# Kernel tuning notes

Hardware: AMD Instinct MI355X
Metric: run time of the kernel (lower is better)

## Reference

```python
import jax, jax.numpy as jnp
import numpy as np

NUM_HEADS = 16
D_MODEL = 1024
NUM_LAYERS = 4
VOCAB = 32000
SEQ_LEN = 1024
BATCH = 4
EPS = 1e-6


def position_embedding(seq_len, d_model):
    pos = jnp.arange(seq_len, dtype=jnp.float32)[:, None]
    i = jnp.arange(d_model, dtype=jnp.float32)[None, :]
    # faithful to source: angle_rates = 1 / (1/10000)^(2*(i//2)/d) = 10000^(2*(i//2)/d)
    angle_rates = jnp.power(10000.0, 2.0 * jnp.floor(i / 2.0) / float(d_model))
    ang = pos * angle_rates  # [S, D]
    return jnp.concatenate([jnp.sin(ang[:, 0::2]), jnp.cos(ang[:, 1::2])], axis=-1)[None]  # [1,S,D]


def layer_norm(x, g, b):
    m = jnp.mean(x, axis=-1, keepdims=True)
    v = jnp.mean(jnp.square(x - m), axis=-1, keepdims=True)
    return (x - m) * jax.lax.rsqrt(v + EPS) * g + b


def setup_inputs() -> dict:
    key = jax.random.key(0)
    ks = jax.random.split(key, 20)
    L, D = NUM_LAYERS, D_MODEL
    s = 0.02
    inp = {
        "x": jax.random.randint(ks[0], (BATCH, SEQ_LEN), 0, VOCAB, dtype=jnp.int32),
        "mask": jnp.zeros((BATCH, 1, 1, SEQ_LEN), dtype=jnp.float32),
        "emb": jax.random.normal(ks[1], (VOCAB, D), dtype=jnp.float32) * s,
        "wq": jax.random.normal(ks[2], (L, D, D), dtype=jnp.float32) * s,
        "bq": jnp.zeros((L, D), dtype=jnp.float32),
        "wk": jax.random.normal(ks[3], (L, D, D), dtype=jnp.float32) * s,
        "bk": jnp.zeros((L, D), dtype=jnp.float32),
        "wv": jax.random.normal(ks[4], (L, D, D), dtype=jnp.float32) * s,
        "bv": jnp.zeros((L, D), dtype=jnp.float32),
        "wo": jax.random.normal(ks[5], (L, D, D), dtype=jnp.float32) * s,
        "bo": jnp.zeros((L, D), dtype=jnp.float32),
        "wf": jax.random.normal(ks[6], (L, D, D), dtype=jnp.float32) * s,
        "bf": jnp.zeros((L, D), dtype=jnp.float32),
        "g1": jnp.ones((L, D), dtype=jnp.float32),
        "b1": jnp.zeros((L, D), dtype=jnp.float32),
        "g2": jnp.ones((L, D), dtype=jnp.float32),
        "b2": jnp.zeros((L, D), dtype=jnp.float32),
    }
    return inp


def encoder_forward(x, mask, emb, wq, bq, wk, bk, wv, bv, wo, bo, wf, bf, g1, b1, g2, b2):
    B, S = x.shape
    D = emb.shape[1]
    H = NUM_HEADS
    dh = D // H
    h = emb[x] * jnp.sqrt(jnp.float32(D))  # [B,S,D]
    h = h + position_embedding(S, D)[:, :S, :]

    def split_heads(t):  # [B,S,D] -> [B,H,S,dh]
        return t.reshape(B, S, H, dh).transpose(0, 2, 1, 3)

    for l in range(wq.shape[0]):
        q = split_heads(h @ wq[l] + bq[l])
        k = split_heads(h @ wk[l] + bk[l])
        v = split_heads(h @ wv[l] + bv[l])
        scores = jnp.einsum("bhqd,bhkd->bhqk", q, k) / jnp.sqrt(jnp.float32(dh))
        scores = scores + mask * -1e9
        w = jax.nn.softmax(scores, axis=-1)
        ctx = jnp.einsum("bhqk,bhkd->bhqd", w, v)  # [B,H,S,dh]
        ctx = ctx.transpose(0, 2, 1, 3).reshape(B, S, D)
        attn_out = ctx @ wo[l] + bo[l]
        h = layer_norm(h + attn_out, g1[l], b1[l])
        ff = h @ wf[l] + bf[l]
        h = layer_norm(h + ff, g2[l], b2[l])
    return h


def reference(x, mask, emb, wq, bq, wk, bk, wv, bv, wo, bo, wf, bf, g1, b1, g2, b2):
    return encoder_forward(x, mask, emb, wq, bq, wk, bk, wv, bv, wo, bo, wf, bf, g1, b1, g2, b2)
```

## Files before the change

### kernel.cpp

```cpp
#include <hip/hip_runtime.h>
#include <hip/hip_bf16.h>
#include <math.h>

typedef __hip_bfloat16 bf16;
typedef unsigned int u32;
typedef __attribute__((ext_vector_type(8))) short short8;
typedef __attribute__((ext_vector_type(4))) float f32x4;


#define ATT_LDK 72
#define PS_LD  72

typedef __attribute__((address_space(3))) u32 lds_u32;
typedef const __attribute__((address_space(1))) u32 glb_u32;
static __device__ __forceinline__ void g2l16(const void* g, void* l) {
    __builtin_amdgcn_global_load_lds((glb_u32*)g, (lds_u32*)l, 16, 0, 0);
}

static __device__ __forceinline__ unsigned short bf16bits(float f) {
    bf16 h = __float2bfloat16(f);
    return *(unsigned short*)&h;
}

__global__ __launch_bounds__(256) void wprep_kernel(
    const float* __restrict__ wq, const float* __restrict__ wk,
    const float* __restrict__ wv, const float* __restrict__ wo,
    const float* __restrict__ wf, bf16* __restrict__ wt_all)
{
    __shared__ bf16 tile[64][ATT_LDK];
    const int z = blockIdx.z;
    const int l = z / 5, f = z % 5;
    const float* src = (f == 0) ? wq : (f == 1) ? wk : (f == 2) ? wv : (f == 3) ? wo : wf;
    src += (size_t)l * 1024 * 1024;
    bf16* dst = wt_all + ((size_t)l * 5 + f) * 1024 * 1024;

    const int k0 = blockIdx.x * 64, n0 = blockIdx.y * 64;
    const int t = threadIdx.x;
#pragma unroll
    for (int rr = 0; rr < 4; ++rr) {
        int slot = t + rr * 256;
        int r = slot >> 4, c = slot & 15;
        float4 v = *(const float4*)(src + (size_t)(k0 + r) * 1024 + n0 + c * 4);
        tile[c * 4 + 0][r] = __float2bfloat16(v.x);
        tile[c * 4 + 1][r] = __float2bfloat16(v.y);
        tile[c * 4 + 2][r] = __float2bfloat16(v.z);
        tile[c * 4 + 3][r] = __float2bfloat16(v.w);
    }
    __syncthreads();
#pragma unroll
    for (int rr = 0; rr < 2; ++rr) {
        int slot = t + rr * 256;
        int n = slot >> 3, c = slot & 7;
        *(uint4*)(dst + (size_t)(n0 + n) * 1024 + k0 + c * 8) = *(const uint4*)&tile[n][c * 8];
    }
}

__global__ void bias_stack_kernel(const float* __restrict__ bq, const float* __restrict__ bk,
                                  const float* __restrict__ bv, float* __restrict__ bqkv,
                                  float* __restrict__ rate)
{
    int i = blockIdx.x * 256 + threadIdx.x;
    if (i < 1024) {
        int m = (i < 512) ? i : (i - 512);
        float ex = (float)(2 * m) * (1.0f / 1024.0f);
        rate[i] = (float)pow(10000.0, (double)ex);
    }
    if (i < 4 * 3072) {
        int l = i / 3072, c = i % 3072;
        int fam = c >> 10, cc = c & 1023;
        const float* s = (fam == 0) ? bq : (fam == 1) ? bk : bv;
        bqkv[i] = s[l * 1024 + cc];
    }
}

__global__ __launch_bounds__(256) void pe_kernel(const float* __restrict__ rate,
                                                 float* __restrict__ pe)
{
    int idx = blockIdx.x * 256 + threadIdx.x;
    int d0 = (idx & 255) * 4;
    int s = idx >> 8;
    float out[4];
#pragma unroll
    for (int j = 0; j < 4; ++j) {
        int d = d0 + j;
        float ang = (float)s * rate[d];
        double a = (double)ang;
        out[j] = (d < 512) ? (float)sin(a) : (float)cos(a);
    }
    *(float4*)(pe + (size_t)s * 1024 + d0) = *(float4*)out;
}

__global__ __launch_bounds__(256) void embed_kernel(
    const int* __restrict__ x, const float* __restrict__ emb,
    const float* __restrict__ pe,
    float* __restrict__ hf, bf16* __restrict__ hb)
{
    int idx = blockIdx.x * 256 + threadIdx.x;
    int d0 = (idx & 255) * 4;
    int row = idx >> 8;
    int s = row & 1023;
    int tok = x[row];
    float4 e = *(const float4*)(emb + (size_t)tok * 1024 + d0);
    float4 p = *(const float4*)(pe + (size_t)s * 1024 + d0);
    float out[4] = {e.x * 32.0f + p.x, e.y * 32.0f + p.y,
                    e.z * 32.0f + p.z, e.w * 32.0f + p.w};
    *(float4*)(hf + (size_t)row * 1024 + d0) = *(float4*)out;
    unsigned short pk[4];
#pragma unroll
    for (int j = 0; j < 4; ++j) pk[j] = bf16bits(out[j]);
    *(uint2*)(hb + (size_t)row * 1024 + d0) = *(uint2*)pk;
}

__global__ __launch_bounds__(256, 3) void gemm_bt_kernel(
    const bf16* __restrict__ A, const bf16* __restrict__ Bt,
    const float* __restrict__ bias,
    bf16* __restrict__ Cb, bf16* __restrict__ VtOut,
    int M, int N, int K)
{
    __shared__ bf16 As[2][128 * 32];
    __shared__ bf16 Bs[2][128 * 32];
    __shared__ bf16 Cst[4][16 * PS_LD];
    const int t = threadIdx.x;
    const int lane = t & 63, wave = t >> 6;
    const int wr = wave >> 1, wc = wave & 1;
    const int lidx = lane & 15, quad = lane >> 4;
    const int m0 = blockIdx.x * 128, n0 = blockIdx.y * 128;

    f32x4 acc[4][4];
#pragma unroll
    for (int i = 0; i < 4; ++i)
#pragma unroll
        for (int j = 0; j < 4; ++j) acc[i][j] = (f32x4){0.f, 0.f, 0.f, 0.f};

    const int r0 = wave * 32;
    const int rloc = lane >> 2;
    const int csw = ((lane & 3) ^ ((lane >> 3) & 3)) * 8;
    const bf16* Abase = A  + (size_t)(m0 + r0 + rloc) * K + csw;
    const bf16* Bbase = Bt + (size_t)(n0 + r0 + rloc) * K + csw;
    const int lofs = r0 * 32;
    const int aslot = (quad ^ ((lidx >> 1) & 3)) * 8;

    g2l16(Abase,                  &As[0][lofs]);
    g2l16(Abase + 16 * (size_t)K, &As[0][lofs + 16 * 32]);
    g2l16(Bbase,                  &Bs[0][lofs]);
    g2l16(Bbase + 16 * (size_t)K, &Bs[0][lofs + 16 * 32]);

    for (int k0 = 0; k0 < K; k0 += 32) {
        __syncthreads();
        const int cur = (k0 >> 5) & 1;
        if (k0 + 32 < K) {
            const int kn = k0 + 32;
            g2l16(Abase + kn,                  &As[cur ^ 1][lofs]);
            g2l16(Abase + kn + 16 * (size_t)K, &As[cur ^ 1][lofs + 16 * 32]);
            g2l16(Bbase + kn,                  &Bs[cur ^ 1][lofs]);
            g2l16(Bbase + kn + 16 * (size_t)K, &Bs[cur ^ 1][lofs + 16 * 32]);
        }

        short8 af[4], bfr[4];
#pragma unroll
        for (int i = 0; i < 4; ++i)
            af[i] = *(const short8*)(&As[cur][(wr * 64 + i * 16 + lidx) * 32 + aslot]);
#pragma unroll
        for (int j = 0; j < 4; ++j)
            bfr[j] = *(const short8*)(&Bs[cur][(wc * 64 + j * 16 + lidx) * 32 + aslot]);
#pragma unroll
        for (int i = 0; i < 4; ++i)
#pragma unroll
            for (int j = 0; j < 4; ++j)
                acc[i][j] = __builtin_amdgcn_mfma_f32_16x16x32_bf16(af[i], bfr[j], acc[i][j], 0, 0, 0);
    }

    float bvj[4];
#pragma unroll
    for (int j = 0; j < 4; ++j)
        bvj[j] = bias ? bias[n0 + wc * 64 + j * 16 + lidx] : 0.0f;

    if (VtOut && n0 >= 2048) {
        const int bidx = m0 >> 10;
        const int s_base = (m0 & 1023) + wr * 64 + quad * 4;
        const int d_base = (n0 - 2048) + wc * 64;
#pragma unroll
        for (int i = 0; i < 4; ++i)
#pragma unroll
            for (int j = 0; j < 4; ++j) {
                unsigned short pk[4];
#pragma unroll
                for (int r = 0; r < 4; ++r)
                    pk[r] = bf16bits(acc[i][j][r] + bvj[j]);
                bf16* dst = VtOut + ((size_t)bidx * 1024 + d_base + j * 16 + lidx) * 1024
                            + s_base + i * 16;
                *(uint2*)dst = *(const uint2*)pk;
            }
    } else {
        const int row16 = lane >> 2, c4 = lane & 3;
#pragma unroll
        for (int i = 0; i < 4; ++i) {
#pragma unroll
            for (int j = 0; j < 4; ++j)
#pragma unroll
                for (int r = 0; r < 4; ++r)
                    Cst[wave][(quad * 4 + r) * PS_LD + j * 16 + lidx] =
                        __float2bfloat16(acc[i][j][r] + bvj[j]);
            bf16* dst = Cb + (size_t)(m0 + wr * 64 + i * 16 + row16) * N + n0 + wc * 64;
            const bf16* srcr = &Cst[wave][row16 * PS_LD];
#pragma unroll
            for (int h = 0; h < 2; ++h)
                *(uint4*)(dst + (c4 + 4 * h) * 8) = *(const uint4*)(srcr + (c4 + 4 * h) * 8);
        }
    }
}

__global__ __launch_bounds__(256, 4) void gemm64_kernel(
    const bf16* __restrict__ A, const bf16* __restrict__ Bt,
    const float* __restrict__ bias, const float* __restrict__ resid,
    float* __restrict__ Cf,
    int M, int N, int K)
{
    __shared__ bf16 As[2][64 * 32];
    __shared__ bf16 Bs[2][128 * 32];
    const int t = threadIdx.x;
    const int lane = t & 63, wave = t >> 6;
    const int wr = wave >> 1, wc = wave & 1;
    const int lidx = lane & 15, quad = lane >> 4;
    const int m0 = blockIdx.x * 64, n0 = blockIdx.y * 128;

    f32x4 acc[2][4];
#pragma unroll
    for (int i = 0; i < 2; ++i)
#pragma unroll
        for (int j = 0; j < 4; ++j) acc[i][j] = (f32x4){0.f, 0.f, 0.f, 0.f};

    const int rloc = lane >> 2;
    const int csw = ((lane & 3) ^ ((lane >> 3) & 3)) * 8;
    const bf16* Abase = A  + (size_t)(m0 + wave * 16 + rloc) * K + csw;
    const bf16* Bbase = Bt + (size_t)(n0 + wave * 32 + rloc) * K + csw;
    const int alofs = wave * 16 * 32;
    const int blofs = wave * 32 * 32;
    const int aslot = (quad ^ ((lidx >> 1) & 3)) * 8;

    g2l16(Abase,                  &As[0][alofs]);
    g2l16(Bbase,                  &Bs[0][blofs]);
    g2l16(Bbase + 16 * (size_t)K, &Bs[0][blofs + 16 * 32]);

    for (int k0 = 0; k0 < K; k0 += 32) {
        __syncthreads();
        const int cur = (k0 >> 5) & 1;
        if (k0 + 32 < K) {
            const int kn = k0 + 32;
            g2l16(Abase + kn,                  &As[cur ^ 1][alofs]);
            g2l16(Bbase + kn,                  &Bs[cur ^ 1][blofs]);
            g2l16(Bbase + kn + 16 * (size_t)K, &Bs[cur ^ 1][blofs + 16 * 32]);
        }

        short8 af[2], bfr[4];
#pragma unroll
        for (int i = 0; i < 2; ++i)
            af[i] = *(const short8*)(&As[cur][(wr * 32 + i * 16 + lidx) * 32 + aslot]);
#pragma unroll
        for (int j = 0; j < 4; ++j)
            bfr[j] = *(const short8*)(&Bs[cur][(wc * 64 + j * 16 + lidx) * 32 + aslot]);
#pragma unroll
        for (int i = 0; i < 2; ++i)
#pragma unroll
            for (int j = 0; j < 4; ++j)
                acc[i][j] = __builtin_amdgcn_mfma_f32_16x16x32_bf16(af[i], bfr[j], acc[i][j], 0, 0, 0);
    }

#pragma unroll
    for (int i = 0; i < 2; ++i)
#pragma unroll
        for (int j = 0; j < 4; ++j) {
            int col = n0 + wc * 64 + j * 16 + lidx;
            float bv = bias[col];
#pragma unroll
            for (int r = 0; r < 4; ++r) {
                int rowg = m0 + wr * 32 + i * 16 + quad * 4 + r;
                Cf[(size_t)rowg * N + col] =
                    acc[i][j][r] + bv + resid[(size_t)rowg * N + col];
            }
        }
}

__global__ __launch_bounds__(512, 4) void attention_kernel(
    const bf16* __restrict__ QKV,
    const bf16* __restrict__ Vt,
    const float* __restrict__ mask,
    bf16* __restrict__ ctx)
{
    __shared__ bf16 Ks[2][64 * 64];
    __shared__ bf16 Vs[2][64 * 64];
    __shared__ bf16 Ps[8][16 * PS_LD];

    const int t = threadIdx.x, lane = t & 63, wave = t >> 6;
    const int quad = lane >> 4, lidx = lane & 15;
    const int b = blockIdx.x >> 4, hh = blockIdx.x & 15;
    const int q0 = blockIdx.y * 128 + wave * 16;

    const int r8 = lane >> 3;
    const int gc = ((lane & 7) ^ r8) * 8;
    const bf16* kg0 = QKV + (size_t)(b * 1024 + wave * 8 + r8) * 3072 + 1024 + hh * 64 + gc;
    const bf16* vg0 = Vt  + (size_t)(b * 1024 + hh * 64 + wave * 8 + r8) * 1024 + gc;
    const int lofs = wave * 8 * 64;

    short8 qf[2];
    {
        const bf16* qp = QKV + (size_t)(b * 1024 + q0 + lidx) * 3072 + hh * 64;
        qf[0] = *(const short8*)(qp + quad * 8);
        qf[1] = *(const short8*)(qp + 32 + quad * 8);
    }

    f32x4 Oacc[4];
#pragma unroll
    for (int nt = 0; nt < 4; ++nt) Oacc[nt] = (f32x4){0.f, 0.f, 0.f, 0.f};
    float psum[4] = {0.f, 0.f, 0.f, 0.f};

    const int fslot = lidx & 7;

    g2l16(kg0, &Ks[0][lofs]);
    g2l16(vg0, &Vs[0][lofs]);

    for (int kt = 0; kt < 16; ++kt) {
        __syncthreads();
        const int cur = kt & 1;
        if (kt < 15) {
            g2l16(kg0 + (size_t)(kt + 1) * 64 * 3072, &Ks[cur ^ 1][lofs]);
            g2l16(vg0 + (kt + 1) * 64,                &Vs[cur ^ 1][lofs]);
        }

        f32x4 sacc[4];
#pragma unroll
        for (int nt = 0; nt < 4; ++nt) sacc[nt] = (f32x4){0.f, 0.f, 0.f, 0.f};
#pragma unroll
        for (int kk = 0; kk < 2; ++kk)
#pragma unroll
            for (int nt = 0; nt < 4; ++nt) {
                short8 kf = *(const short8*)(&Ks[cur][(nt * 16 + lidx) * 64 + (((kk * 4 + quad) ^ fslot) * 8)]);
                sacc[nt] = __builtin_amdgcn_mfma_f32_16x16x32_bf16(qf[kk], kf, sacc[nt], 0, 0, 0);
            }

#pragma unroll
        for (int nt = 0; nt < 4; ++nt) {
            float mv = mask[b * 1024 + kt * 64 + nt * 16 + lidx] * -1e9f;
#pragma unroll
            for (int r = 0; r < 4; ++r) {
                float p = __expf(sacc[nt][r] * 0.125f + mv);
                sacc[nt][r] = p;
                psum[r] += p;
            }
        }

#pragma unroll
        for (int nt = 0; nt < 4; ++nt)
#pragma unroll
            for (int r = 0; r < 4; ++r)
                Ps[wave][(quad * 4 + r) * PS_LD + nt * 16 + lidx] = __float2bfloat16(sacc[nt][r]);

#pragma unroll
        for (int kk = 0; kk < 2; ++kk) {
            short8 pf = *(const short8*)(&Ps[wave][lidx * PS_LD + kk * 32 + quad * 8]);
#pragma unroll
            for (int nt = 0; nt < 4; ++nt) {
                short8 vf = *(const short8*)(&Vs[cur][(nt * 16 + lidx) * 64 + (((kk * 4 + quad) ^ fslot) * 8)]);
                Oacc[nt] = __builtin_amdgcn_mfma_f32_16x16x32_bf16(pf, vf, Oacc[nt], 0, 0, 0);
            }
        }
    }

#pragma unroll
    for (int off = 1; off < 16; off <<= 1)
#pragma unroll
        for (int r = 0; r < 4; ++r)
            psum[r] += __shfl_xor(psum[r], off, 64);
    float linv[4];
#pragma unroll
    for (int r = 0; r < 4; ++r) linv[r] = 1.0f / psum[r];

#pragma unroll
    for (int nt = 0; nt < 4; ++nt)
#pragma unroll
        for (int r = 0; r < 4; ++r)
            Ps[wave][(quad * 4 + r) * PS_LD + nt * 16 + lidx] = __float2bfloat16(Oacc[nt][r] * linv[r]);

    const int row16 = lane >> 2, c4 = lane & 3;
    bf16* dst = ctx + (size_t)(b * 1024 + q0 + row16) * 1024 + hh * 64;
    const bf16* srcr = &Ps[wave][row16 * PS_LD];
#pragma unroll
    for (int h = 0; h < 2; ++h)
        *(uint4*)(dst + (c4 + 4 * h) * 8) = *(const uint4*)(srcr + (c4 + 4 * h) * 8);
}

__global__ __launch_bounds__(256) void add_ln_kernel(
    const float* __restrict__ x,
    const float* __restrict__ g, const float* __restrict__ b,
    float* __restrict__ outf, bf16* __restrict__ outb)
{
    __shared__ float red[4];
    const int row = blockIdx.x;
    const int t = threadIdx.x;
    const int c0 = t * 4;
    float4 xv = *(const float4*)(x + (size_t)row * 1024 + c0);
    float v[4] = {xv.x, xv.y, xv.z, xv.w};
    float s = v[0] + v[1] + v[2] + v[3];
#pragma unroll
    for (int off = 1; off < 64; off <<= 1) s += __shfl_xor(s, off, 64);
    if ((t & 63) == 0) red[t >> 6] = s;
    __syncthreads();
    float mean = (red[0] + red[1] + red[2] + red[3]) * (1.0f / 1024.0f);
    float sq = 0.f;
#pragma unroll
    for (int i = 0; i < 4; ++i) { float d = v[i] - mean; sq += d * d; }
#pragma unroll
    for (int off = 1; off < 64; off <<= 1) sq += __shfl_xor(sq, off, 64);
    __syncthreads();
    if ((t & 63) == 0) red[t >> 6] = sq;
    __syncthreads();
    float var = (red[0] + red[1] + red[2] + red[3]) * (1.0f / 1024.0f);
    float rs = rsqrtf(var + 1e-6f);
    float4 gv = *(const float4*)(g + c0);
    float4 bv = *(const float4*)(b + c0);
    float gg[4] = {gv.x, gv.y, gv.z, gv.w}, bb[4] = {bv.x, bv.y, bv.z, bv.w};
    float o[4];
    unsigned short pk[4];
#pragma unroll
    for (int i = 0; i < 4; ++i) {
        o[i] = (v[i] - mean) * rs * gg[i] + bb[i];
        pk[i] = bf16bits(o[i]);
    }
    *(float4*)(outf + (size_t)row * 1024 + c0) = *(float4*)o;
    *(uint2*)(outb + (size_t)row * 1024 + c0) = *(uint2*)pk;
}

extern "C" void kernel_launch(void* const* d_in, const int* in_sizes, int n_in,
                              void* d_out, int out_size, void* d_ws, size_t ws_size,
                              hipStream_t stream)
{
    const int*   x    = (const int*)d_in[0];
    const float* mask = (const float*)d_in[1];
    const float* emb  = (const float*)d_in[2];
    const float* wq   = (const float*)d_in[3];
    const float* bq   = (const float*)d_in[4];
    const float* wk   = (const float*)d_in[5];
    const float* bk   = (const float*)d_in[6];
    const float* wv   = (const float*)d_in[7];
    const float* bv   = (const float*)d_in[8];
    const float* wo   = (const float*)d_in[9];
    const float* bo   = (const float*)d_in[10];
    const float* wf   = (const float*)d_in[11];
    const float* bfp  = (const float*)d_in[12];
    const float* g1   = (const float*)d_in[13];
    const float* b1   = (const float*)d_in[14];
    const float* g2   = (const float*)d_in[15];
    const float* b2   = (const float*)d_in[16];

    char* ws = (char*)d_ws;
    float* h_f  = (float*)ws;                 ws += 4096ull * 1024 * 4;
    bf16*  h_b  = (bf16*)ws;                  ws += 4096ull * 1024 * 2;
    bf16*  qkv  = (bf16*)ws;                  ws += 4096ull * 3072 * 2;
    bf16*  vt   = (bf16*)ws;                  ws += 4096ull * 1024 * 2;
    bf16*  ctx  = (bf16*)ws;                  ws += 4096ull * 1024 * 2;
    bf16*  wt   = (bf16*)ws;                  ws += 20ull * 1024 * 1024 * 2;
    float* pe   = (float*)ws;                 ws += 1024ull * 1024 * 4;
    float* bqkv = (float*)ws;                 ws += 4ull * 3072 * 4;
    float* rate = (float*)ws;                 ws += 1024ull * 4;
    float* delta = (float*)qkv;

    wprep_kernel<<<dim3(16, 16, 20), 256, 0, stream>>>(wq, wk, wv, wo, wf, wt);
    bias_stack_kernel<<<dim3(48), 256, 0, stream>>>(bq, bk, bv, bqkv, rate);
    pe_kernel<<<dim3(1024), 256, 0, stream>>>(rate, pe);
    embed_kernel<<<dim3(4096), 256, 0, stream>>>(x, emb, pe, h_f, h_b);

    for (int l = 0; l < 4; ++l) {
        bf16* wt_l = wt + (size_t)l * 5 * 1024 * 1024;
        gemm_bt_kernel<<<dim3(32, 24), 256, 0, stream>>>(
            h_b, wt_l, bqkv + l * 3072, qkv, vt, 4096, 3072, 1024);
        attention_kernel<<<dim3(64, 8), 512, 0, stream>>>(qkv, vt, mask, ctx);
        gemm64_kernel<<<dim3(64, 8), 256, 0, stream>>>(
            ctx, wt_l + 3ull * 1024 * 1024, bo + l * 1024, h_f, delta, 4096, 1024, 1024);
        add_ln_kernel<<<dim3(4096), 256, 0, stream>>>(
            delta, g1 + l * 1024, b1 + l * 1024, h_f, h_b);
        gemm64_kernel<<<dim3(64, 8), 256, 0, stream>>>(
            h_b, wt_l + 4ull * 1024 * 1024, bfp + l * 1024, h_f, delta, 4096, 1024, 1024);
        float* outf = (l == 3) ? (float*)d_out : h_f;
        add_ln_kernel<<<dim3(4096), 256, 0, stream>>>(
            delta, g2 + l * 1024, b2 + l * 1024, outf, h_b);
    }
    (void)in_sizes; (void)n_in; (void)out_size; (void)ws_size;
}
```

Baseline: 771.8 us.

## Give each attention wave two query tiles, stage mask in LDS, pack two LN rows per block

The attention kernel moves from 8 waves of 16 query rows to 4 waves of 32 query rows. Each K/V fragment read from LDS now feeds two MFMAs, which halves LDS fragment traffic per unit of compute but raises register pressure. The mask is scaled once into a bf16 LDS array instead of being reloaded from global memory every tile. add_ln now processes two rows per 512-thread block, halving the block count.

```diff
diff --git a/kernel.cpp b/kernel.cpp
--- a/kernel.cpp
+++ b/kernel.cpp
@@ -281,7 +281,7 @@
         }
 }
 
-__global__ __launch_bounds__(512, 4) void attention_kernel(
+__global__ __launch_bounds__(256, 2) void attention_kernel(
     const bf16* __restrict__ QKV,
     const bf16* __restrict__ Vt,
     const float* __restrict__ mask,
@@ -289,79 +289,103 @@
 {
     __shared__ bf16 Ks[2][64 * 64];
     __shared__ bf16 Vs[2][64 * 64];
-    __shared__ bf16 Ps[8][16 * PS_LD];
+    __shared__ bf16 Ps[4][32 * PS_LD];
+    __shared__ bf16 Ms[1024];
 
     const int t = threadIdx.x, lane = t & 63, wave = t >> 6;
     const int quad = lane >> 4, lidx = lane & 15;
     const int b = blockIdx.x >> 4, hh = blockIdx.x & 15;
-    const int q0 = blockIdx.y * 128 + wave * 16;
+    const int q0 = blockIdx.y * 128 + wave * 32;
 
     const int r8 = lane >> 3;
     const int gc = ((lane & 7) ^ r8) * 8;
-    const bf16* kg0 = QKV + (size_t)(b * 1024 + wave * 8 + r8) * 3072 + 1024 + hh * 64 + gc;
-    const bf16* vg0 = Vt  + (size_t)(b * 1024 + hh * 64 + wave * 8 + r8) * 1024 + gc;
-    const int lofs = wave * 8 * 64;
-
-    short8 qf[2];
-    {
-        const bf16* qp = QKV + (size_t)(b * 1024 + q0 + lidx) * 3072 + hh * 64;
-        qf[0] = *(const short8*)(qp + quad * 8);
-        qf[1] = *(const short8*)(qp + 32 + quad * 8);
-    }
-
-    f32x4 Oacc[4];
-#pragma unroll
-    for (int nt = 0; nt < 4; ++nt) Oacc[nt] = (f32x4){0.f, 0.f, 0.f, 0.f};
-    float psum[4] = {0.f, 0.f, 0.f, 0.f};
+    const bf16* kg0 = QKV + (size_t)(b * 1024 + wave * 16 + r8) * 3072 + 1024 + hh * 64 + gc;
+    const bf16* vg0 = Vt  + (size_t)(b * 1024 + hh * 64 + wave * 16 + r8) * 1024 + gc;
+    const int lofs = wave * 16 * 64;
+
+#pragma unroll
+    for (int i = 0; i < 4; ++i)
+        Ms[t + i * 256] = __float2bfloat16(mask[b * 1024 + t + i * 256] * -1e9f);
+
+    short8 qf[2][2];
+#pragma unroll
+    for (int qs = 0; qs < 2; ++qs) {
+        const bf16* qp = QKV + (size_t)(b * 1024 + q0 + qs * 16 + lidx) * 3072 + hh * 64;
+        qf[qs][0] = *(const short8*)(qp + quad * 8);
+        qf[qs][1] = *(const short8*)(qp + 32 + quad * 8);
+    }
+
+    f32x4 Oacc[2][4];
+#pragma unroll
+    for (int qs = 0; qs < 2; ++qs)
+#pragma unroll
+        for (int nt = 0; nt < 4; ++nt) Oacc[qs][nt] = (f32x4){0.f, 0.f, 0.f, 0.f};
+    float psum[2][4] = {{0.f, 0.f, 0.f, 0.f}, {0.f, 0.f, 0.f, 0.f}};
 
     const int fslot = lidx & 7;
 
-    g2l16(kg0, &Ks[0][lofs]);
-    g2l16(vg0, &Vs[0][lofs]);
+    g2l16(kg0,            &Ks[0][lofs]);
+    g2l16(kg0 + 8 * 3072, &Ks[0][lofs + 8 * 64]);
+    g2l16(vg0,            &Vs[0][lofs]);
+    g2l16(vg0 + 8 * 1024, &Vs[0][lofs + 8 * 64]);
 
     for (int kt = 0; kt < 16; ++kt) {
         __syncthreads();
         const int cur = kt & 1;
         if (kt < 15) {
-            g2l16(kg0 + (size_t)(kt + 1) * 64 * 3072, &Ks[cur ^ 1][lofs]);
-            g2l16(vg0 + (kt + 1) * 64,                &Vs[cur ^ 1][lofs]);
-        }
-
-        f32x4 sacc[4];
-#pragma unroll
-        for (int nt = 0; nt < 4; ++nt) sacc[nt] = (f32x4){0.f, 0.f, 0.f, 0.f};
+            const bf16* kg = kg0 + (size_t)(kt + 1) * 64 * 3072;
+            const bf16* vg = vg0 + (kt + 1) * 64;
+            g2l16(kg,            &Ks[cur ^ 1][lofs]);
+            g2l16(kg + 8 * 3072, &Ks[cur ^ 1][lofs + 8 * 64]);
+            g2l16(vg,            &Vs[cur ^ 1][lofs]);
+            g2l16(vg + 8 * 1024, &Vs[cur ^ 1][lofs + 8 * 64]);
+        }
+
+        f32x4 sacc[2][4];
+#pragma unroll
+        for (int qs = 0; qs < 2; ++qs)
+#pragma unroll
+            for (int nt = 0; nt < 4; ++nt) sacc[qs][nt] = (f32x4){0.f, 0.f, 0.f, 0.f};
 #pragma unroll
         for (int kk = 0; kk < 2; ++kk)
 #pragma unroll
             for (int nt = 0; nt < 4; ++nt) {
                 short8 kf = *(const short8*)(&Ks[cur][(nt * 16 + lidx) * 64 + (((kk * 4 + quad) ^ fslot) * 8)]);
-                sacc[nt] = __builtin_amdgcn_mfma_f32_16x16x32_bf16(qf[kk], kf, sacc[nt], 0, 0, 0);
+                sacc[0][nt] = __builtin_amdgcn_mfma_f32_16x16x32_bf16(qf[0][kk], kf, sacc[0][nt], 0, 0, 0);
+                sacc[1][nt] = __builtin_amdgcn_mfma_f32_16x16x32_bf16(qf[1][kk], kf, sacc[1][nt], 0, 0, 0);
             }
 
 #pragma unroll
         for (int nt = 0; nt < 4; ++nt) {
-            float mv = mask[b * 1024 + kt * 64 + nt * 16 + lidx] * -1e9f;
-#pragma unroll
-            for (int r = 0; r < 4; ++r) {
-                float p = __expf(sacc[nt][r] * 0.125f + mv);
-                sacc[nt][r] = p;
-                psum[r] += p;
-            }
-        }
-
-#pragma unroll
-        for (int nt = 0; nt < 4; ++nt)
-#pragma unroll
-            for (int r = 0; r < 4; ++r)
-                Ps[wave][(quad * 4 + r) * PS_LD + nt * 16 + lidx] = __float2bfloat16(sacc[nt][r]);
+            float mv = __bfloat162float(Ms[kt * 64 + nt * 16 + lidx]);
+#pragma unroll
+            for (int qs = 0; qs < 2; ++qs)
+#pragma unroll
+                for (int r = 0; r < 4; ++r) {
+                    float p = __expf(sacc[qs][nt][r] * 0.125f + mv);
+                    sacc[qs][nt][r] = p;
+                    psum[qs][r] += p;
+                }
+        }
+
+#pragma unroll
+        for (int qs = 0; qs < 2; ++qs)
+#pragma unroll
+            for (int nt = 0; nt < 4; ++nt)
+#pragma unroll
+                for (int r = 0; r < 4; ++r)
+                    Ps[wave][(qs * 16 + quad * 4 + r) * PS_LD + nt * 16 + lidx] =
+                        __float2bfloat16(sacc[qs][nt][r]);
 
 #pragma unroll
         for (int kk = 0; kk < 2; ++kk) {
-            short8 pf = *(const short8*)(&Ps[wave][lidx * PS_LD + kk * 32 + quad * 8]);
+            short8 pf0 = *(const short8*)(&Ps[wave][(lidx) * PS_LD + kk * 32 + quad * 8]);
+            short8 pf1 = *(const short8*)(&Ps[wave][(16 + lidx) * PS_LD + kk * 32 + quad * 8]);
 #pragma unroll
             for (int nt = 0; nt < 4; ++nt) {
                 short8 vf = *(const short8*)(&Vs[cur][(nt * 16 + lidx) * 64 + (((kk * 4 + quad) ^ fslot) * 8)]);
-                Oacc[nt] = __builtin_amdgcn_mfma_f32_16x16x32_bf16(pf, vf, Oacc[nt], 0, 0, 0);
+                Oacc[0][nt] = __builtin_amdgcn_mfma_f32_16x16x32_bf16(pf0, vf, Oacc[0][nt], 0, 0, 0);
+                Oacc[1][nt] = __builtin_amdgcn_mfma_f32_16x16x32_bf16(pf1, vf, Oacc[1][nt], 0, 0, 0);
             }
         }
     }
@@ -369,52 +393,65 @@
 #pragma unroll
     for (int off = 1; off < 16; off <<= 1)
 #pragma unroll
-        for (int r = 0; r < 4; ++r)
-            psum[r] += __shfl_xor(psum[r], off, 64);
-    float linv[4];
-#pragma unroll
-    for (int r = 0; r < 4; ++r) linv[r] = 1.0f / psum[r];
-
-#pragma unroll
-    for (int nt = 0; nt < 4; ++nt)
-#pragma unroll
-        for (int r = 0; r < 4; ++r)
-            Ps[wave][(quad * 4 + r) * PS_LD + nt * 16 + lidx] = __float2bfloat16(Oacc[nt][r] * linv[r]);
+        for (int qs = 0; qs < 2; ++qs)
+#pragma unroll
+            for (int r = 0; r < 4; ++r)
+                psum[qs][r] += __shfl_xor(psum[qs][r], off, 64);
+    float linv[2][4];
+#pragma unroll
+    for (int qs = 0; qs < 2; ++qs)
+#pragma unroll
+        for (int r = 0; r < 4; ++r) linv[qs][r] = 1.0f / psum[qs][r];
+
+#pragma unroll
+    for (int qs = 0; qs < 2; ++qs)
+#pragma unroll
+        for (int nt = 0; nt < 4; ++nt)
+#pragma unroll
+            for (int r = 0; r < 4; ++r)
+                Ps[wave][(qs * 16 + quad * 4 + r) * PS_LD + nt * 16 + lidx] =
+                    __float2bfloat16(Oacc[qs][nt][r] * linv[qs][r]);
 
     const int row16 = lane >> 2, c4 = lane & 3;
-    bf16* dst = ctx + (size_t)(b * 1024 + q0 + row16) * 1024 + hh * 64;
-    const bf16* srcr = &Ps[wave][row16 * PS_LD];
-#pragma unroll
-    for (int h = 0; h < 2; ++h)
-        *(uint4*)(dst + (c4 + 4 * h) * 8) = *(const uint4*)(srcr + (c4 + 4 * h) * 8);
-}
-
-__global__ __launch_bounds__(256) void add_ln_kernel(
+#pragma unroll
+    for (int qs = 0; qs < 2; ++qs) {
+        bf16* dst = ctx + (size_t)(b * 1024 + q0 + qs * 16 + row16) * 1024 + hh * 64;
+        const bf16* srcr = &Ps[wave][(qs * 16 + row16) * PS_LD];
+#pragma unroll
+        for (int h = 0; h < 2; ++h)
+            *(uint4*)(dst + (c4 + 4 * h) * 8) = *(const uint4*)(srcr + (c4 + 4 * h) * 8);
+    }
+}
+
+__global__ __launch_bounds__(512) void add_ln_kernel(
     const float* __restrict__ x,
     const float* __restrict__ g, const float* __restrict__ b,
     float* __restrict__ outf, bf16* __restrict__ outb)
 {
-    __shared__ float red[4];
-    const int row = blockIdx.x;
-    const int t = threadIdx.x;
+    __shared__ float red[8];
+    const int half = threadIdx.x >> 8;
+    const int row = blockIdx.x * 2 + half;
+    const int t = threadIdx.x & 255;
+    const int wv = threadIdx.x >> 6;
+    const int rb = half * 4;
     const int c0 = t * 4;
     float4 xv = *(const float4*)(x + (size_t)row * 1024 + c0);
     float v[4] = {xv.x, xv.y, xv.z, xv.w};
     float s = v[0] + v[1] + v[2] + v[3];
 #pragma unroll
     for (int off = 1; off < 64; off <<= 1) s += __shfl_xor(s, off, 64);
-    if ((t & 63) == 0) red[t >> 6] = s;
+    if ((threadIdx.x & 63) == 0) red[wv] = s;
     __syncthreads();
-    float mean = (red[0] + red[1] + red[2] + red[3]) * (1.0f / 1024.0f);
+    float mean = (red[rb] + red[rb + 1] + red[rb + 2] + red[rb + 3]) * (1.0f / 1024.0f);
     float sq = 0.f;
 #pragma unroll
     for (int i = 0; i < 4; ++i) { float d = v[i] - mean; sq += d * d; }
 #pragma unroll
     for (int off = 1; off < 64; off <<= 1) sq += __shfl_xor(sq, off, 64);
     __syncthreads();
-    if ((t & 63) == 0) red[t >> 6] = sq;
+    if ((threadIdx.x & 63) == 0) red[wv] = sq;
     __syncthreads();
-    float var = (red[0] + red[1] + red[2] + red[3]) * (1.0f / 1024.0f);
+    float var = (red[rb] + red[rb + 1] + red[rb + 2] + red[rb + 3]) * (1.0f / 1024.0f);
     float rs = rsqrtf(var + 1e-6f);
     float4 gv = *(const float4*)(g + c0);
     float4 bv = *(const float4*)(b + c0);
@@ -473,15 +510,15 @@
         bf16* wt_l = wt + (size_t)l * 5 * 1024 * 1024;
         gemm_bt_kernel<<<dim3(32, 24), 256, 0, stream>>>(
             h_b, wt_l, bqkv + l * 3072, qkv, vt, 4096, 3072, 1024);
-        attention_kernel<<<dim3(64, 8), 512, 0, stream>>>(qkv, vt, mask, ctx);
+        attention_kernel<<<dim3(64, 8), 256, 0, stream>>>(qkv, vt, mask, ctx);
         gemm64_kernel<<<dim3(64, 8), 256, 0, stream>>>(
             ctx, wt_l + 3ull * 1024 * 1024, bo + l * 1024, h_f, delta, 4096, 1024, 1024);
-        add_ln_kernel<<<dim3(4096), 256, 0, stream>>>(
+        add_ln_kernel<<<dim3(2048), 512, 0, stream>>>(
             delta, g1 + l * 1024, b1 + l * 1024, h_f, h_b);
         gemm64_kernel<<<dim3(64, 8), 256, 0, stream>>>(
             h_b, wt_l + 4ull * 1024 * 1024, bfp + l * 1024, h_f, delta, 4096, 1024, 1024);
         float* outf = (l == 3) ? (float*)d_out : h_f;
-        add_ln_kernel<<<dim3(4096), 256, 0, stream>>>(
+        add_ln_kernel<<<dim3(2048), 512, 0, stream>>>(
             delta, g2 + l * 1024, b2 + l * 1024, outf, h_b);
     }
     (void)in_sizes; (void)n_in; (void)out_size; (void)ws_size;
```

Result: no change. 760.6 us (-1.5%).
